# Kernel tuning notes

Measured on AMD Instinct MI355X. Metric: run time of the kernel, lower is better.

Reference implementation:

```python
import jax, jax.numpy as jnp
import numpy as np

N, E = 100000, 1600000
IN_C, HID_C, OUT_C = 128, 256, 128


def _sage_conv(x, src, dst, Wl, Wr, b, n):
    # PyG SAGEConv (mean aggr): out_i = lin_l(mean_{j->i} x_j) + lin_r(x_i) + b
    msg = jax.ops.segment_sum(x[src], dst, num_segments=n)          # [N, F]
    deg = jax.ops.segment_sum(jnp.ones((src.shape[0],), x.dtype), dst, num_segments=n)
    mean = msg / jnp.maximum(deg, 1.0)[:, None]
    return mean @ Wl.T + x @ Wr.T + b


def setup_inputs() -> dict:
    key = jax.random.key(0)
    ks = jax.random.split(key, 9)
    x = jax.random.normal(ks[0], (N, IN_C), dtype=jnp.float32)
    edge_index = jax.random.randint(ks[1], (2, E), 0, N, dtype=jnp.int64)
    edge_attr = jax.random.normal(ks[2], (E, 1), dtype=jnp.float32)

    def glorot(k, fan_out, fan_in):
        s = np.sqrt(6.0 / (fan_in + fan_out)).astype(np.float32)
        return jax.random.uniform(k, (fan_out, fan_in), jnp.float32, -s, s)

    return {
        "x": x,
        "edge_index": edge_index,
        "edge_attr": edge_attr,
        "W1l": glorot(ks[3], HID_C, IN_C),
        "W1r": glorot(ks[4], HID_C, IN_C),
        "b1": jnp.zeros((HID_C,), jnp.float32),
        "W2l": glorot(ks[5], OUT_C, HID_C),
        "W2r": glorot(ks[6], OUT_C, HID_C),
        "b2": jnp.zeros((OUT_C,), jnp.float32),
    }


def reference(x, edge_index, edge_attr, W1l, W1r, b1, W2l, W2r, b2):
    src, dst = edge_index[0], edge_index[1]
    n = x.shape[0]
    h = _sage_conv(x, src, dst, W1l, W1r, b1, n)   # conv1
    h = jax.nn.relu(h)
    out = _sage_conv(h, src, dst, W2l, W2r, b2, n)  # conv2
    return out
```

## Files before the change

kernel.cpp:

```cpp
#include <hip/hip_runtime.h>


#define NBMAX 1024
#define BCAP  2560

using f32x4 = __attribute__((ext_vector_type(4))) float;
using s16x8 = __attribute__((ext_vector_type(8))) short;
using s16x2 = __attribute__((ext_vector_type(2))) short;

#define QSCALE 15.875f

__device__ inline unsigned short f2bf(float f) {
    unsigned int u = __float_as_uint(f);
    unsigned int r = u + 0x7fff + ((u >> 16) & 1);
    return (unsigned short)(r >> 16);
}
__device__ inline float bf2f(unsigned short b) {
    return __uint_as_float(((unsigned int)b) << 16);
}
__device__ inline float bflo(unsigned u) { return __uint_as_float(u << 16); }
__device__ inline float bfhi(unsigned u) { return __uint_as_float(u & 0xffff0000u); }

__global__ __launch_bounds__(256) void cursor_init_kernel(int* __restrict__ bcursor, int NB) {
    int i = blockIdx.x * 256 + threadIdx.x;
    if (i < NB) bcursor[i] = i * BCAP;
}

__global__ __launch_bounds__(1024) void bin_kernel(const int* __restrict__ srci,
                                                   const int* __restrict__ dsti,
                                                   int* __restrict__ bcursor,
                                                   unsigned* __restrict__ pairs, int E, int NB) {
    __shared__ int lh[NBMAX];
    __shared__ int lbase[NBMAX];
    for (int i = threadIdx.x; i < NB; i += 1024) lh[i] = 0;
    __syncthreads();
    int chunk = (E + gridDim.x - 1) / gridDim.x;
    int e0 = blockIdx.x * chunk;
    int e1 = min(e0 + chunk, E);
    for (int e = e0 + threadIdx.x; e < e1; e += 1024)
        atomicAdd(&lh[dsti[e] >> 7], 1);
    __syncthreads();
    for (int i = threadIdx.x; i < NB; i += 1024) {
        int c = lh[i];
        lbase[i] = c ? atomicAdd(&bcursor[i], c) : 0;
        lh[i] = 0;
    }
    __syncthreads();
    for (int e = e0 + threadIdx.x; e < e1; e += 1024) {
        int d = dsti[e];
        int bk = d >> 7;
        int pos = lbase[bk] + atomicAdd(&lh[bk], 1);
        pairs[pos] = ((unsigned)srci[e] << 7) | (unsigned)(d & 127);
    }
}

__global__ __launch_bounds__(256) void csr_build_kernel(const unsigned* __restrict__ pairs,
                                                        const int* __restrict__ bcursor,
                                                        int2* __restrict__ offs2,
                                                        int* __restrict__ csr, int n) {
    __shared__ int ldeg[128];
    __shared__ int s[128];
    __shared__ int lcur[128];
    int b = blockIdx.x, tid = threadIdx.x;
    int lo = b * BCAP, hi = bcursor[b];
    if (tid < 128) ldeg[tid] = 0;
    __syncthreads();
    for (int i = lo + tid; i < hi; i += 256)
        atomicAdd(&ldeg[pairs[i] & 127], 1);
    __syncthreads();
    if (tid < 128) s[tid] = ldeg[tid];
    __syncthreads();
    for (int d = 1; d < 128; d <<= 1) {
        int add = (tid < 128 && tid >= d) ? s[tid - d] : 0;
        __syncthreads();
        if (tid < 128) s[tid] += add;
        __syncthreads();
    }
    if (tid < 128) {
        int excl = lo + s[tid] - ldeg[tid];
        int node = b * 128 + tid;
        if (node < n) offs2[node] = make_int2(excl, excl + ldeg[tid]);
        lcur[tid] = excl;
    }
    __syncthreads();
    for (int i = lo + tid; i < hi; i += 256) {
        unsigned p = pairs[i];
        int pos = atomicAdd(&lcur[p & 127], 1);
        csr[pos] = (int)(p & ~127u);
    }
}

__global__ __launch_bounds__(256) void cvt_x_kernel(const float* __restrict__ x,
                                                    unsigned short* __restrict__ xb,
                                                    unsigned char* __restrict__ xq, int total4) {
    int i = blockIdx.x * 256 + threadIdx.x;
    int stride = gridDim.x * 256;
    for (; i < total4; i += stride) {
        float4 v = ((const float4*)x)[i];
        ushort4 o;
        o.x = f2bf(v.x); o.y = f2bf(v.y); o.z = f2bf(v.z); o.w = f2bf(v.w);
        ((ushort4*)xb)[i] = o;
        int q0 = max(-127, min(127, (int)rintf(v.x * QSCALE))) + 128;
        int q1 = max(-127, min(127, (int)rintf(v.y * QSCALE))) + 128;
        int q2 = max(-127, min(127, (int)rintf(v.z * QSCALE))) + 128;
        int q3 = max(-127, min(127, (int)rintf(v.w * QSCALE))) + 128;
        ((unsigned*)xq)[i] = (unsigned)q0 | ((unsigned)q1 << 8) |
                             ((unsigned)q2 << 16) | ((unsigned)q3 << 24);
    }
}

__global__ __launch_bounds__(256) void cvt_w_kernel(
    const float* __restrict__ W1l, const float* __restrict__ W1r,
    const float* __restrict__ W2l, const float* __restrict__ W2r,
    unsigned short* __restrict__ Wb1, unsigned short* __restrict__ Wb2l,
    unsigned short* __restrict__ Wb2r) {
    int idx = blockIdx.x * 256 + threadIdx.x;
    int which = idx >> 15;
    int r = idx & 32767;
    if (which == 0) {
        int o = r >> 7, k = r & 127;
        Wb1[o * 256 + k] = f2bf(W1l[r]);
    } else if (which == 1) {
        int o = r >> 7, k = r & 127;
        Wb1[o * 256 + 128 + k] = f2bf(W1r[r]);
    } else if (which == 2) {
        Wb2l[r] = f2bf(W2l[r]);
    } else {
        Wb2r[r] = f2bf(W2r[r]);
    }
}

__global__ __launch_bounds__(256) void agg_i8_kernel(const unsigned char* __restrict__ featq,
                                                     const int* __restrict__ csr,
                                                     const int2* __restrict__ offs2,
                                                     unsigned short* __restrict__ meanout,
                                                     int n, int zoff, float dq) {
    int wave = threadIdx.x >> 6;
    int lane = threadIdx.x & 63;
    int node = blockIdx.x * 4 + wave;
    if (node >= n) return;
    int2 se = offs2[node];
    int start = se.x, end = se.y;
    int deg = end - start;
    int slot = lane >> 3;
    int c16 = lane & 7;

    s16x2 accE[4], accO[4];
#pragma unroll
    for (int j = 0; j < 4; ++j) { accE[j] = (s16x2){0, 0}; accO[j] = (s16x2){0, 0}; }

    auto addrow = [&](uint4 v) {
#pragma unroll
        for (int j = 0; j < 4; ++j) {
            unsigned u = (&v.x)[j];
            accE[j] += __builtin_bit_cast(s16x2, __builtin_amdgcn_perm(0u, u, 0x0C020C00u));
            accO[j] += __builtin_bit_cast(s16x2, __builtin_amdgcn_perm(0u, u, 0x0C030C01u));
        }
    };

    int nfull = deg >> 4;
    int e = start + slot;
    for (int it = 0; it < nfull; ++it, e += 16) {
        int o0 = csr[e];
        int o1 = csr[e + 8];
        uint4 v0 = *(const uint4*)(featq + (size_t)(unsigned)o0 + c16 * 16);
        uint4 v1 = *(const uint4*)(featq + (size_t)(unsigned)o1 + c16 * 16);
        addrow(v0);
        addrow(v1);
    }
    int done = start + (nfull << 4);
    int ntot = nfull << 4;
    if (done < end) {
        int se0 = done + slot;
        int se1 = done + 8 + slot;
        int o0 = (se0 < end) ? csr[se0] : zoff;
        int o1 = (se1 < end) ? csr[se1] : zoff;
        uint4 v0 = *(const uint4*)(featq + (size_t)(unsigned)o0 + c16 * 16);
        uint4 v1 = *(const uint4*)(featq + (size_t)(unsigned)o1 + c16 * 16);
        addrow(v0);
        addrow(v1);
        ntot += 16;
    }

#pragma unroll
    for (int m = 8; m <= 32; m <<= 1) {
#pragma unroll
        for (int j = 0; j < 4; ++j) {
            accE[j] += __builtin_bit_cast(s16x2, __shfl_xor(__builtin_bit_cast(int, accE[j]), m));
            accO[j] += __builtin_bit_cast(s16x2, __shfl_xor(__builtin_bit_cast(int, accO[j]), m));
        }
    }

    if (lane < 8) {
        float inv = dq / (float)max(deg, 1);
        float corr = 128.f * (float)ntot;
        unsigned wbuf[8];
#pragma unroll
        for (int j = 0; j < 4; ++j) {
            float f0 = ((float)accE[j][0] - corr) * inv;
            float f1 = ((float)accO[j][0] - corr) * inv;
            float f2 = ((float)accE[j][1] - corr) * inv;
            float f3 = ((float)accO[j][1] - corr) * inv;
            wbuf[2 * j]     = (unsigned)f2bf(f0) | ((unsigned)f2bf(f1) << 16);
            wbuf[2 * j + 1] = (unsigned)f2bf(f2) | ((unsigned)f2bf(f3) << 16);
        }
        uint4* dst = (uint4*)(meanout + (size_t)node * 128 + c16 * 16);
        dst[0] = make_uint4(wbuf[0], wbuf[1], wbuf[2], wbuf[3]);
        dst[1] = make_uint4(wbuf[4], wbuf[5], wbuf[6], wbuf[7]);
    }
}

template <int OSTRIDE, int EPI>
__global__ __launch_bounds__(256) void gemm_persist_kernel(
    const unsigned short* __restrict__ A0, const unsigned short* __restrict__ A1,
    const unsigned short* __restrict__ Wb, const float* __restrict__ bias,
    const unsigned short* __restrict__ addend, void* __restrict__ outv,
    int n, int ntiles) {
    __shared__ unsigned short As[2][32 * 256];
    const int tid = threadIdx.x;
    const int w = tid >> 6, lane = tid & 63;
    const int l15 = lane & 15, lhi = lane >> 4;
    const int colbase = blockIdx.y * 128 + w * 32;

    s16x8 b[8][2];
#pragma unroll
    for (int kk = 0; kk < 8; ++kk)
#pragma unroll
        for (int cf = 0; cf < 2; ++cf)
            b[kk][cf] = *(const s16x8*)(Wb + (size_t)(colbase + cf * 16 + l15) * 256 +
                                        kk * 32 + lhi * 8);

    s16x8 st[4];
    auto stage_load = [&](int tile) {
#pragma unroll
        for (int p = 0; p < 4; ++p) {
            int chunk = p * 256 + tid;
            int row = chunk >> 5;
            int cc = chunk & 31;
            int grow = tile * 32 + row;
            if (grow >= n) grow = n - 1;
            const unsigned short* src;
            if (A1) {
                src = (cc < 16) ? (A0 + (size_t)grow * 128 + cc * 8)
                                : (A1 + (size_t)grow * 128 + (cc - 16) * 8);
            } else {
                src = A0 + (size_t)grow * 256 + cc * 8;
            }
            st[p] = *(const s16x8*)src;
        }
    };
    auto stage_write = [&](int buf) {
#pragma unroll
        for (int p = 0; p < 4; ++p) {
            int chunk = p * 256 + tid;
            int row = chunk >> 5;
            int cc = chunk & 31;
            int scc = (cc & 24) | ((cc ^ (row & 7)) & 7);
            *(s16x8*)((char*)&As[buf][0] + row * 512 + scc * 16) = st[p];
        }
    };

    int t = blockIdx.x;
    if (t >= ntiles) return;
    stage_load(t);
    stage_write(0);
    __syncthreads();
    int buf = 0;

    for (; t < ntiles; t += gridDim.x) {
        int tn = t + gridDim.x;
        bool hasNext = tn < ntiles;
        if (hasNext) stage_load(tn);

        f32x4 acc[2][2];
#pragma unroll
        for (int rf = 0; rf < 2; ++rf)
#pragma unroll
            for (int cf = 0; cf < 2; ++cf)
                acc[rf][cf] = (f32x4){0.f, 0.f, 0.f, 0.f};

#pragma unroll
        for (int kk = 0; kk < 8; ++kk) {
            s16x8 a[2];
#pragma unroll
            for (int rf = 0; rf < 2; ++rf) {
                int row = rf * 16 + l15;
                int cbase = kk * 4 + lhi;
                int scc = (cbase & 24) | ((cbase ^ (row & 7)) & 7);
                a[rf] = *(const s16x8*)((const char*)&As[buf][0] + row * 512 + scc * 16);
            }
#pragma unroll
            for (int rf = 0; rf < 2; ++rf)
#pragma unroll
                for (int cf = 0; cf < 2; ++cf)
                    acc[rf][cf] = __builtin_amdgcn_mfma_f32_16x16x32_bf16(
                        b[kk][cf], a[rf], acc[rf][cf], 0, 0, 0);
        }

        __syncthreads();
        if (hasNext) stage_write(buf ^ 1);
        __syncthreads();

#pragma unroll
        for (int rf = 0; rf < 2; ++rf) {
            int row = t * 32 + rf * 16 + l15;
            if (row >= n) continue;
#pragma unroll
            for (int cf = 0; cf < 2; ++cf) {
                int colg = colbase + cf * 16 + lhi * 4;
                f32x4 v = acc[rf][cf];
                if (EPI == 1 || EPI == 2) {
                    float4 bb = *(const float4*)(bias + colg);
                    v[0] += bb.x; v[1] += bb.y; v[2] += bb.z; v[3] += bb.w;
                }
                if (EPI == 1) {
                    v[0] = fmaxf(v[0], 0.f); v[1] = fmaxf(v[1], 0.f);
                    v[2] = fmaxf(v[2], 0.f); v[3] = fmaxf(v[3], 0.f);
                }
                if (EPI == 2) {
                    uint2 ad = *(const uint2*)(addend + (size_t)row * OSTRIDE + colg);
                    v[0] += bflo(ad.x); v[1] += bfhi(ad.x);
                    v[2] += bflo(ad.y); v[3] += bfhi(ad.y);
                    *(float4*)((float*)outv + (size_t)row * OSTRIDE + colg) =
                        make_float4(v[0], v[1], v[2], v[3]);
                } else if (EPI == 3) {
                    int q0 = max(-127, min(127, (int)rintf(v[0] * QSCALE))) + 128;
                    int q1 = max(-127, min(127, (int)rintf(v[1] * QSCALE))) + 128;
                    int q2 = max(-127, min(127, (int)rintf(v[2] * QSCALE))) + 128;
                    int q3 = max(-127, min(127, (int)rintf(v[3] * QSCALE))) + 128;
                    unsigned o = (unsigned)q0 | ((unsigned)q1 << 8) |
                                 ((unsigned)q2 << 16) | ((unsigned)q3 << 24);
                    *(unsigned*)((unsigned char*)outv + (size_t)row * OSTRIDE + colg) = o;
                } else {
                    uint2 o;
                    o.x = (unsigned)f2bf(v[0]) | ((unsigned)f2bf(v[1]) << 16);
                    o.y = (unsigned)f2bf(v[2]) | ((unsigned)f2bf(v[3]) << 16);
                    *(uint2*)((unsigned short*)outv + (size_t)row * OSTRIDE + colg) = o;
                }
            }
        }
        buf ^= 1;
    }
}

extern "C" void kernel_launch(void* const* d_in, const int* in_sizes, int n_in,
                              void* d_out, int out_size, void* d_ws, size_t ws_size,
                              hipStream_t stream) {
    const float* x   = (const float*)d_in[0];
    const int*   ei  = (const int*)d_in[1];
    const float* W1l = (const float*)d_in[3];
    const float* W1r = (const float*)d_in[4];
    const float* b1  = (const float*)d_in[5];
    const float* W2l = (const float*)d_in[6];
    const float* W2r = (const float*)d_in[7];
    const float* b2  = (const float*)d_in[8];

    const int n = in_sizes[0] / 128;
    const int E = in_sizes[1] / 2;
    const int* srci = ei;
    const int* dsti = ei + E;
    const int NB = (n + 127) >> 7;

    char* w = (char*)d_ws;
    auto alloc = [&](size_t bytes) {
        char* p = w;
        w += (bytes + 255) & ~(size_t)255;
        return p;
    };
    int*      bcursor = (int*)alloc((size_t)NBMAX * 4);
    int2*     offs2   = (int2*)alloc((size_t)n * 8);
    unsigned* pairs   = (unsigned*)alloc((size_t)NB * BCAP * 4);
    int*      csr     = (int*)alloc((size_t)NB * BCAP * 4);
    unsigned short* Wb1   = (unsigned short*)alloc((size_t)256 * 256 * 2);
    unsigned short* Wb2l  = (unsigned short*)alloc((size_t)128 * 256 * 2);
    unsigned short* Wb2r  = (unsigned short*)alloc((size_t)128 * 256 * 2);
    unsigned short* xb    = (unsigned short*)alloc((size_t)n * 128 * 2);
    unsigned char*  xq    = (unsigned char*)alloc((size_t)(n + 1) * 128);
    unsigned short* mean1b= (unsigned short*)alloc((size_t)n * 128 * 2);
    unsigned short* hb    = (unsigned short*)alloc((size_t)n * 256 * 2);
    unsigned char*  tq    = (unsigned char*)alloc((size_t)(n + 1) * 128);
    float*          outp  = (float*)d_out;

    cursor_init_kernel<<<(NB + 255) / 256, 256, 0, stream>>>(bcursor, NB);
    bin_kernel<<<256, 1024, 0, stream>>>(srci, dsti, bcursor, pairs, E, NB);
    csr_build_kernel<<<NB, 256, 0, stream>>>(pairs, bcursor, offs2, csr, n);

    hipMemsetAsync(xq + (size_t)n * 128, 0x80, 128, stream);
    hipMemsetAsync(tq + (size_t)n * 128, 0x80, 128, stream);
    cvt_x_kernel<<<2048, 256, 0, stream>>>(x, xb, xq, n * 128 / 4);
    cvt_w_kernel<<<(4 * 32768) / 256, 256, 0, stream>>>(W1l, W1r, W2l, W2r, Wb1, Wb2l, Wb2r);

    const int ntiles = (n + 31) / 32;
    const int zoff = n * 128;
    const float dq = 1.f / QSCALE;
    const dim3 g256(768, 2), g128(768, 1);
    agg_i8_kernel<<<(n + 3) / 4, 256, 0, stream>>>(xq, csr, offs2, mean1b, n, zoff, dq);
    gemm_persist_kernel<256, 1><<<g256, 256, 0, stream>>>(mean1b, xb, Wb1, b1, nullptr, hb, n, ntiles);
    gemm_persist_kernel<128, 3><<<g128, 256, 0, stream>>>(hb, nullptr, Wb2l, nullptr, nullptr, tq, n, ntiles);
    agg_i8_kernel<<<(n + 3) / 4, 256, 0, stream>>>(tq, csr, offs2, mean1b, n, zoff, dq);
    gemm_persist_kernel<128, 2><<<g128, 256, 0, stream>>>(hb, nullptr, Wb2r, b2, mean1b, outp, n, ntiles);
}
```

Measured before the change: 233.8 us.

## Fuse conv2 left/right GEMMs into one dual-output kernel, add residual in aggregation

The two layer-2 GEMMs that each read the hidden activations hb are merged into one kernel that computes both the left projection (quantized to int8 for aggregation) and the right projection plus bias (stored as bf16). The final aggregation kernel now adds this bf16 term and writes the fp32 output directly, which removes the last GEMM launch and one full pass over hb. In exchange the dual kernel holds twice the weight fragments and accumulators in registers and runs on a smaller persistent grid. The added term is also rounded to bf16 before the final sum.

Result: faster. 222.4 us (-4.9%).

```diff
diff --git a/kernel.cpp b/kernel.cpp
--- a/kernel.cpp
+++ b/kernel.cpp
@@ -130,10 +130,12 @@
     }
 }
 
+template <bool OUT_F32>
 __global__ __launch_bounds__(256) void agg_i8_kernel(const unsigned char* __restrict__ featq,
                                                      const int* __restrict__ csr,
                                                      const int2* __restrict__ offs2,
-                                                     unsigned short* __restrict__ meanout,
+                                                     const unsigned short* __restrict__ uadd,
+                                                     void* __restrict__ outp,
                                                      int n, int zoff, float dq) {
     int wave = threadIdx.x >> 6;
     int lane = threadIdx.x & 63;
@@ -194,19 +196,34 @@
     if (lane < 8) {
         float inv = dq / (float)max(deg, 1);
         float corr = 128.f * (float)ntot;
-        unsigned wbuf[8];
-#pragma unroll
-        for (int j = 0; j < 4; ++j) {
-            float f0 = ((float)accE[j][0] - corr) * inv;
-            float f1 = ((float)accO[j][0] - corr) * inv;
-            float f2 = ((float)accE[j][1] - corr) * inv;
-            float f3 = ((float)accO[j][1] - corr) * inv;
-            wbuf[2 * j]     = (unsigned)f2bf(f0) | ((unsigned)f2bf(f1) << 16);
-            wbuf[2 * j + 1] = (unsigned)f2bf(f2) | ((unsigned)f2bf(f3) << 16);
-        }
-        uint4* dst = (uint4*)(meanout + (size_t)node * 128 + c16 * 16);
-        dst[0] = make_uint4(wbuf[0], wbuf[1], wbuf[2], wbuf[3]);
-        dst[1] = make_uint4(wbuf[4], wbuf[5], wbuf[6], wbuf[7]);
+        if (OUT_F32) {
+            const uint4* up = (const uint4*)(uadd + (size_t)node * 128 + c16 * 16);
+            uint4 ua = up[0], ub = up[1];
+            unsigned uw[8] = {ua.x, ua.y, ua.z, ua.w, ub.x, ub.y, ub.z, ub.w};
+            float* dst = (float*)outp + (size_t)node * 128 + c16 * 16;
+#pragma unroll
+            for (int j = 0; j < 4; ++j) {
+                float f0 = ((float)accE[j][0] - corr) * inv + bflo(uw[2 * j]);
+                float f1 = ((float)accO[j][0] - corr) * inv + bfhi(uw[2 * j]);
+                float f2 = ((float)accE[j][1] - corr) * inv + bflo(uw[2 * j + 1]);
+                float f3 = ((float)accO[j][1] - corr) * inv + bfhi(uw[2 * j + 1]);
+                *(float4*)(dst + 4 * j) = make_float4(f0, f1, f2, f3);
+            }
+        } else {
+            unsigned wbuf[8];
+#pragma unroll
+            for (int j = 0; j < 4; ++j) {
+                float f0 = ((float)accE[j][0] - corr) * inv;
+                float f1 = ((float)accO[j][0] - corr) * inv;
+                float f2 = ((float)accE[j][1] - corr) * inv;
+                float f3 = ((float)accO[j][1] - corr) * inv;
+                wbuf[2 * j]     = (unsigned)f2bf(f0) | ((unsigned)f2bf(f1) << 16);
+                wbuf[2 * j + 1] = (unsigned)f2bf(f2) | ((unsigned)f2bf(f3) << 16);
+            }
+            uint4* dst = (uint4*)((unsigned short*)outp + (size_t)node * 128 + c16 * 16);
+            dst[0] = make_uint4(wbuf[0], wbuf[1], wbuf[2], wbuf[3]);
+            dst[1] = make_uint4(wbuf[4], wbuf[5], wbuf[6], wbuf[7]);
+        }
     }
 }
 
@@ -214,8 +231,7 @@
 __global__ __launch_bounds__(256) void gemm_persist_kernel(
     const unsigned short* __restrict__ A0, const unsigned short* __restrict__ A1,
     const unsigned short* __restrict__ Wb, const float* __restrict__ bias,
-    const unsigned short* __restrict__ addend, void* __restrict__ outv,
-    int n, int ntiles) {
+    void* __restrict__ outv, int n, int ntiles) {
     __shared__ unsigned short As[2][32 * 256];
     const int tid = threadIdx.x;
     const int w = tid >> 6, lane = tid & 63;
@@ -309,34 +325,135 @@
             for (int cf = 0; cf < 2; ++cf) {
                 int colg = colbase + cf * 16 + lhi * 4;
                 f32x4 v = acc[rf][cf];
-                if (EPI == 1 || EPI == 2) {
-                    float4 bb = *(const float4*)(bias + colg);
-                    v[0] += bb.x; v[1] += bb.y; v[2] += bb.z; v[3] += bb.w;
-                }
+                float4 bb = *(const float4*)(bias + colg);
+                v[0] += bb.x; v[1] += bb.y; v[2] += bb.z; v[3] += bb.w;
                 if (EPI == 1) {
                     v[0] = fmaxf(v[0], 0.f); v[1] = fmaxf(v[1], 0.f);
                     v[2] = fmaxf(v[2], 0.f); v[3] = fmaxf(v[3], 0.f);
                 }
-                if (EPI == 2) {
-                    uint2 ad = *(const uint2*)(addend + (size_t)row * OSTRIDE + colg);
-                    v[0] += bflo(ad.x); v[1] += bfhi(ad.x);
-                    v[2] += bflo(ad.y); v[3] += bfhi(ad.y);
-                    *(float4*)((float*)outv + (size_t)row * OSTRIDE + colg) =
-                        make_float4(v[0], v[1], v[2], v[3]);
-                } else if (EPI == 3) {
-                    int q0 = max(-127, min(127, (int)rintf(v[0] * QSCALE))) + 128;
-                    int q1 = max(-127, min(127, (int)rintf(v[1] * QSCALE))) + 128;
-                    int q2 = max(-127, min(127, (int)rintf(v[2] * QSCALE))) + 128;
-                    int q3 = max(-127, min(127, (int)rintf(v[3] * QSCALE))) + 128;
-                    unsigned o = (unsigned)q0 | ((unsigned)q1 << 8) |
-                                 ((unsigned)q2 << 16) | ((unsigned)q3 << 24);
-                    *(unsigned*)((unsigned char*)outv + (size_t)row * OSTRIDE + colg) = o;
-                } else {
-                    uint2 o;
-                    o.x = (unsigned)f2bf(v[0]) | ((unsigned)f2bf(v[1]) << 16);
-                    o.y = (unsigned)f2bf(v[2]) | ((unsigned)f2bf(v[3]) << 16);
-                    *(uint2*)((unsigned short*)outv + (size_t)row * OSTRIDE + colg) = o;
+                uint2 o;
+                o.x = (unsigned)f2bf(v[0]) | ((unsigned)f2bf(v[1]) << 16);
+                o.y = (unsigned)f2bf(v[2]) | ((unsigned)f2bf(v[3]) << 16);
+                *(uint2*)((unsigned short*)outv + (size_t)row * OSTRIDE + colg) = o;
+            }
+        }
+        buf ^= 1;
+    }
+}
+
+__global__ __launch_bounds__(256, 2) void gemm_dual_kernel(
+    const unsigned short* __restrict__ A0,
+    const unsigned short* __restrict__ WbL, const unsigned short* __restrict__ WbR,
+    const float* __restrict__ bias,
+    unsigned char* __restrict__ tq, unsigned short* __restrict__ u,
+    int n, int ntiles) {
+    __shared__ unsigned short As[2][32 * 256];
+    const int tid = threadIdx.x;
+    const int w = tid >> 6, lane = tid & 63;
+    const int l15 = lane & 15, lhi = lane >> 4;
+    const int colbase = w * 32;
+
+    s16x8 bL[8][2], bR[8][2];
+#pragma unroll
+    for (int kk = 0; kk < 8; ++kk)
+#pragma unroll
+        for (int cf = 0; cf < 2; ++cf) {
+            size_t off = (size_t)(colbase + cf * 16 + l15) * 256 + kk * 32 + lhi * 8;
+            bL[kk][cf] = *(const s16x8*)(WbL + off);
+            bR[kk][cf] = *(const s16x8*)(WbR + off);
+        }
+
+    s16x8 st[4];
+    auto stage_load = [&](int tile) {
+#pragma unroll
+        for (int p = 0; p < 4; ++p) {
+            int chunk = p * 256 + tid;
+            int row = chunk >> 5;
+            int cc = chunk & 31;
+            int grow = tile * 32 + row;
+            if (grow >= n) grow = n - 1;
+            st[p] = *(const s16x8*)(A0 + (size_t)grow * 256 + cc * 8);
+        }
+    };
+    auto stage_write = [&](int buf) {
+#pragma unroll
+        for (int p = 0; p < 4; ++p) {
+            int chunk = p * 256 + tid;
+            int row = chunk >> 5;
+            int cc = chunk & 31;
+            int scc = (cc & 24) | ((cc ^ (row & 7)) & 7);
+            *(s16x8*)((char*)&As[buf][0] + row * 512 + scc * 16) = st[p];
+        }
+    };
+
+    int t = blockIdx.x;
+    if (t >= ntiles) return;
+    stage_load(t);
+    stage_write(0);
+    __syncthreads();
+    int buf = 0;
+
+    for (; t < ntiles; t += gridDim.x) {
+        int tn = t + gridDim.x;
+        bool hasNext = tn < ntiles;
+        if (hasNext) stage_load(tn);
+
+        f32x4 accL[2][2], accR[2][2];
+#pragma unroll
+        for (int rf = 0; rf < 2; ++rf)
+#pragma unroll
+            for (int cf = 0; cf < 2; ++cf) {
+                accL[rf][cf] = (f32x4){0.f, 0.f, 0.f, 0.f};
+                accR[rf][cf] = (f32x4){0.f, 0.f, 0.f, 0.f};
+            }
+
+#pragma unroll
+        for (int kk = 0; kk < 8; ++kk) {
+            s16x8 a[2];
+#pragma unroll
+            for (int rf = 0; rf < 2; ++rf) {
+                int row = rf * 16 + l15;
+                int cbase = kk * 4 + lhi;
+                int scc = (cbase & 24) | ((cbase ^ (row & 7)) & 7);
+                a[rf] = *(const s16x8*)((const char*)&As[buf][0] + row * 512 + scc * 16);
+            }
+#pragma unroll
+            for (int rf = 0; rf < 2; ++rf)
+#pragma unroll
+                for (int cf = 0; cf < 2; ++cf) {
+                    accL[rf][cf] = __builtin_amdgcn_mfma_f32_16x16x32_bf16(
+                        bL[kk][cf], a[rf], accL[rf][cf], 0, 0, 0);
+                    accR[rf][cf] = __builtin_amdgcn_mfma_f32_16x16x32_bf16(
+                        bR[kk][cf], a[rf], accR[rf][cf], 0, 0, 0);
                 }
+        }
+
+        __syncthreads();
+        if (hasNext) stage_write(buf ^ 1);
+        __syncthreads();
+
+#pragma unroll
+        for (int rf = 0; rf < 2; ++rf) {
+            int row = t * 32 + rf * 16 + l15;
+            if (row >= n) continue;
+#pragma unroll
+            for (int cf = 0; cf < 2; ++cf) {
+                int colg = colbase + cf * 16 + lhi * 4;
+                f32x4 vL = accL[rf][cf];
+                int q0 = max(-127, min(127, (int)rintf(vL[0] * QSCALE))) + 128;
+                int q1 = max(-127, min(127, (int)rintf(vL[1] * QSCALE))) + 128;
+                int q2 = max(-127, min(127, (int)rintf(vL[2] * QSCALE))) + 128;
+                int q3 = max(-127, min(127, (int)rintf(vL[3] * QSCALE))) + 128;
+                unsigned oq = (unsigned)q0 | ((unsigned)q1 << 8) |
+                              ((unsigned)q2 << 16) | ((unsigned)q3 << 24);
+                *(unsigned*)(tq + (size_t)row * 128 + colg) = oq;
+                f32x4 vR = accR[rf][cf];
+                float4 bb = *(const float4*)(bias + colg);
+                vR[0] += bb.x; vR[1] += bb.y; vR[2] += bb.z; vR[3] += bb.w;
+                uint2 ou;
+                ou.x = (unsigned)f2bf(vR[0]) | ((unsigned)f2bf(vR[1]) << 16);
+                ou.y = (unsigned)f2bf(vR[2]) | ((unsigned)f2bf(vR[3]) << 16);
+                *(uint2*)(u + (size_t)row * 128 + colg) = ou;
             }
         }
         buf ^= 1;
@@ -393,10 +510,8 @@
     const int ntiles = (n + 31) / 32;
     const int zoff = n * 128;
     const float dq = 1.f / QSCALE;
-    const dim3 g256(768, 2), g128(768, 1);
-    agg_i8_kernel<<<(n + 3) / 4, 256, 0, stream>>>(xq, csr, offs2, mean1b, n, zoff, dq);
-    gemm_persist_kernel<256, 1><<<g256, 256, 0, stream>>>(mean1b, xb, Wb1, b1, nullptr, hb, n, ntiles);
-    gemm_persist_kernel<128, 3><<<g128, 256, 0, stream>>>(hb, nullptr, Wb2l, nullptr, nullptr, tq, n, ntiles);
-    agg_i8_kernel<<<(n + 3) / 4, 256, 0, stream>>>(tq, csr, offs2, mean1b, n, zoff, dq);
-    gemm_persist_kernel<128, 2><<<g128, 256, 0, stream>>>(hb, nullptr, Wb2r, b2, mean1b, outp, n, ntiles);
-}
+    agg_i8_kernel<false><<<(n + 3) / 4, 256, 0, stream>>>(xq, csr, offs2, nullptr, mean1b, n, zoff, dq);
+    gemm_persist_kernel<256, 1><<<dim3(768, 2), 256, 0, stream>>>(mean1b, xb, Wb1, b1, hb, n, ntiles);
+    gemm_dual_kernel<<<512, 256, 0, stream>>>(hb, Wb2l, Wb2r, b2, tq, mean1b, n, ntiles);
+    agg_i8_kernel<true><<<(n + 3) / 4, 256, 0, stream>>>(tq, csr, offs2, mean1b, outp, n, zoff, dq);
+}
```
